# Performance work log

Hardware: AMD Instinct MI355X
Metric: run time of the kernel (lower is better)

The kernel has to match this reference:

```python
import jax, jax.numpy as jnp
import numpy as np

M, K, N = 8192, 4096, 4096
INT8_MAX = 127.0


def setup_inputs() -> dict:
    key = jax.random.key(0)
    k1, k2, k3, k4 = jax.random.split(key, 4)
    inp = jax.random.normal(k1, (M, K), dtype=jnp.float32)
    # int8 weight [out_features, in_features]
    weight = jax.random.randint(k2, (N, K), -128, 128, dtype=jnp.int32).astype(jnp.int8)
    # per-output-channel dequant scale
    weight_scale = jax.random.uniform(k3, (N,), dtype=jnp.float32, minval=1e-3, maxval=1e-2)
    bias = jax.random.normal(k4, (N,), dtype=jnp.float32) * 0.01
    return {"input": inp, "weight": weight, "weight_scale": weight_scale, "bias": bias}


def reference(input, weight, weight_scale, bias):
    # Dynamic per-token symmetric int8 quantization (scaled_int8_quant with
    # scale=None, azp=None, symmetric=True): scale_a = max|x| / 127 per row.
    absmax = jnp.max(jnp.abs(input), axis=-1, keepdims=True)  # [M, 1]
    scale_a = jnp.where(absmax > 0, absmax / INT8_MAX, jnp.float32(1.0))
    q = jnp.clip(jnp.round(input / scale_a), -128, 127).astype(jnp.int8)  # [M, K]
    # and per-column (weight_scale) dequant, plus bias, in input dtype.
    acc = jnp.matmul(q.astype(jnp.int32), weight.T.astype(jnp.int32))  # [M, N] int32
    out = acc.astype(jnp.float32) * scale_a * weight_scale[None, :] + bias[None, :]
    return out.astype(input.dtype)
```

## Files before the change

kernel.cpp:

```cpp
#include <hip/hip_runtime.h>
#include <cstdint>

typedef __attribute__((ext_vector_type(4))) int int32x4;
typedef __attribute__((ext_vector_type(16))) int int32x16;

#define GLOBAL_AS __attribute__((address_space(1)))
#define LDS_AS    __attribute__((address_space(3)))

__global__ __launch_bounds__(256) void pack_w(
    const int* __restrict__ w32, uint32_t* __restrict__ w8_as_u32)
{
    const size_t i = (size_t)blockIdx.x * 256 + threadIdx.x;
    const int4 v = ((const int4*)w32)[i];
    w8_as_u32[i] = (v.x & 0xff) | ((v.y & 0xff) << 8) |
                   ((v.z & 0xff) << 16) | ((uint32_t)(v.w & 0xff) << 24);
}

__global__ __launch_bounds__(256) void quant_rows(
    const float* __restrict__ in, int8_t* __restrict__ q,
    float* __restrict__ sa, int K)
{
    const int row = blockIdx.x;
    const float4* rp = (const float4*)(in + (size_t)row * K);
    const int t = threadIdx.x;

    float amax = 0.f;
    float4 v[4];
#pragma unroll
    for (int i = 0; i < 4; ++i) {
        v[i] = rp[t + (i << 8)];
        amax = fmaxf(amax,
               fmaxf(fmaxf(fabsf(v[i].x), fabsf(v[i].y)),
                     fmaxf(fabsf(v[i].z), fabsf(v[i].w))));
    }

#pragma unroll
    for (int off = 32; off; off >>= 1)
        amax = fmaxf(amax, __shfl_xor(amax, off));
    __shared__ float smax[4];
    if ((t & 63) == 0) smax[t >> 6] = amax;
    __syncthreads();
    amax = fmaxf(fmaxf(smax[0], smax[1]), fmaxf(smax[2], smax[3]));

    const float scale = (amax > 0.f) ? (amax / 127.f) : 1.f;
    if (t == 0) sa[row] = scale;
    const float rs = 1.f / scale;

    int* qrow = (int*)(q + (size_t)row * K);
#pragma unroll
    for (int i = 0; i < 4; ++i) {
        int a = __float2int_rn(v[i].x * rs);
        int b = __float2int_rn(v[i].y * rs);
        int c = __float2int_rn(v[i].z * rs);
        int d = __float2int_rn(v[i].w * rs);
        a = max(-128, min(127, a));
        b = max(-128, min(127, b));
        c = max(-128, min(127, c));
        d = max(-128, min(127, d));
        qrow[t + (i << 8)] = (a & 0xff) | ((b & 0xff) << 8) |
                             ((c & 0xff) << 16) | ((d & 0xff) << 24);
    }
}

__device__ __forceinline__ void async_load16(const int8_t* g, int8_t* lds) {
    __builtin_amdgcn_global_load_lds((const GLOBAL_AS char*)g,
                                     (LDS_AS char*)lds, 16, 0, 0);
}

__global__ __launch_bounds__(256, 1) void w8a8_gemm(
    const int8_t* __restrict__ Aq, const int8_t* __restrict__ W,
    const float* __restrict__ sa, const float* __restrict__ wsc,
    const float* __restrict__ bias, float* __restrict__ out,
    int M, int N, int K)
{
    __shared__ int8_t lds[4 * 32768];

    const int NB = N >> 8;
    const int nwg = gridDim.x;
    const int cpx = nwg >> 3;
    const int wg = (blockIdx.x & 7) * cpx + (blockIdx.x >> 3);
    const int bm = wg / NB, bn = wg % NB;

    const int t = threadIdx.x;
    const int lane = t & 63, wid = t >> 6;
    const int wr = wid >> 1, wc = wid & 1;
    const int l31 = lane & 31, h = lane >> 5;
    const int pswz = ((lane >> 1) ^ (lane >> 3)) & 3;

    const int srow = t >> 2;
    const int scol = (((t & 3) ^ ((t >> 3) & 3) ^ ((t >> 5) & 3)) << 4);
    const int8_t* gA = Aq + ((size_t)bm * 256 + srow) * (size_t)K + scol;
    const int8_t* gB = W  + ((size_t)bn * 256 + srow) * (size_t)K + scol;
    const size_t rstep = (size_t)64 * K;
    const size_t hstep = (size_t)128 * K;
    int8_t* ldsw = &lds[t * 16];

    auto stage = [&](int ring, int kbyte, int c) {
        const int8_t* s0 = (c < 2 ? gA : gB) + (size_t)(c & 1) * hstep + kbyte;
        int8_t* d0 = ldsw + ring * 32768 + (c >> 1) * 16384 + (c & 1) * 8192;
        async_load16(s0, d0);
        async_load16(s0 + rstep, d0 + 4096);
    };

    const int aoff = wr * 8192 + l31 * 64;
    const int boff = 16384 + wc * 8192 + l31 * 64;
    const int cs0 = ((0 + h) ^ pswz) << 4;
    const int cs1 = ((2 + h) ^ pswz) << 4;

    int32x16 acc[4][4];
#pragma unroll
    for (int m = 0; m < 4; ++m)
#pragma unroll
        for (int n = 0; n < 4; ++n)
#pragma unroll
            for (int rgi = 0; rgi < 16; ++rgi)
                acc[m][n][rgi] = 0;

    const int NT = K >> 6;

#pragma unroll
    for (int c = 0; c < 4; ++c) stage(0, 0, c);
#pragma unroll
    for (int c = 0; c < 4; ++c) stage(1, 64, c);
    asm volatile("s_waitcnt vmcnt(8)" ::: "memory");
    asm volatile("s_barrier" ::: "memory");

    for (int g = 0; g < NT; ++g) {
        const int rbase = (g & 3) * 32768;
        const int sring = (g + 2) & 3;
        const int skb = (g + 2) << 6;
        const bool do_stage = (g + 2) < NT;

        int32x4 a0[4], b0[4], a1[4], b1[4];
#pragma unroll
        for (int m = 0; m < 4; ++m)
            a0[m] = *(const int32x4*)&lds[rbase + aoff + m * 2048 + cs0];
#pragma unroll
        for (int n = 0; n < 4; ++n)
            b0[n] = *(const int32x4*)&lds[rbase + boff + n * 2048 + cs0];

        if (do_stage) {
#pragma unroll
            for (int c = 0; c < 4; ++c) stage(sring, skb, c);
        }

#pragma unroll
        for (int m = 0; m < 4; ++m)
            a1[m] = *(const int32x4*)&lds[rbase + aoff + m * 2048 + cs1];
#pragma unroll
        for (int n = 0; n < 4; ++n)
            b1[n] = *(const int32x4*)&lds[rbase + boff + n * 2048 + cs1];

#pragma unroll
        for (int m = 0; m < 4; ++m)
#pragma unroll
            for (int n = 0; n < 4; ++n)
                acc[m][n] = __builtin_amdgcn_mfma_i32_32x32x32_i8(
                    a0[m], b0[n], acc[m][n], 0, 0, 0);
#pragma unroll
        for (int m = 0; m < 4; ++m)
#pragma unroll
            for (int n = 0; n < 4; ++n)
                acc[m][n] = __builtin_amdgcn_mfma_i32_32x32x32_i8(
                    a1[m], b1[n], acc[m][n], 0, 0, 0);

        if (g < NT - 2)
            asm volatile("s_waitcnt vmcnt(8)" ::: "memory");
        else
            asm volatile("s_waitcnt vmcnt(0)" ::: "memory");
        asm volatile("s_barrier" ::: "memory");
    }

    const int col0 = bn * 256 + wc * 128 + l31;
    const int row00 = bm * 256 + wr * 128 + 4 * h;

#pragma unroll
    for (int m = 0; m < 4; ++m) {
        float sv[16];
#pragma unroll
        for (int rgi = 0; rgi < 16; ++rgi)
            sv[rgi] = sa[row00 + m * 32 + (rgi & 3) + 8 * (rgi >> 2)];
#pragma unroll
        for (int n = 0; n < 4; ++n) {
            const int col = col0 + n * 32;
            const float wn = wsc[col];
            const float bb = bias[col];
#pragma unroll
            for (int rgi = 0; rgi < 16; ++rgi) {
                const int row = row00 + m * 32 + (rgi & 3) + 8 * (rgi >> 2);
                out[(size_t)row * N + col] =
                    (float)acc[m][n][rgi] * sv[rgi] * wn + bb;
            }
        }
    }
}

extern "C" void kernel_launch(void* const* d_in, const int* in_sizes, int n_in,
                              void* d_out, int out_size, void* d_ws, size_t ws_size,
                              hipStream_t stream) {
    const float* inp  = (const float*)d_in[0];
    const int*   w32  = (const int*)d_in[1];
    const float* wsc  = (const float*)d_in[2];
    const float* bias = (const float*)d_in[3];
    float* out = (float*)d_out;

    const int N = in_sizes[2];
    const int K = in_sizes[1] / N;
    const int M = in_sizes[0] / K;

    int8_t* q  = (int8_t*)d_ws;
    float*  sa = (float*)((char*)d_ws + (size_t)M * K);
    int8_t* w8 = (int8_t*)((char*)d_ws + (size_t)M * K + (size_t)M * 4 + 256);

    const size_t nw4 = ((size_t)N * K) / 4;
    pack_w<<<(int)(nw4 / 256), 256, 0, stream>>>(w32, (uint32_t*)w8);

    quant_rows<<<M, 256, 0, stream>>>(inp, q, sa, K);

    const int nwg = (M / 256) * (N / 256);
    w8a8_gemm<<<nwg, 256, 0, stream>>>(q, w8, sa, wsc, bias, out, M, N, K);
}
```

Baseline: 195.7 us.

## Switch GEMM to double-buffered 128-K groups with conflict-free LDS layout

The 4-slot ring of 64-byte K tiles with XOR-swizzled LDS layout is replaced by a 2-slot double buffer that stages 128 bytes of K per group. The LDS layout is reorganised so each lane reads a contiguous 16-byte chunk (lane*16), which removes the swizzle arithmetic and aims for bank-conflict-free reads. Each barrier now covers twice the MFMA work, so there is less synchronisation overhead. In exchange, prefetch depth drops to one group and each iteration waits for all outstanding loads (vmcnt(0)), which could expose memory latency.

Result: slower. 243.9 us (+24.6%).

```diff
diff --git a/kernel.cpp b/kernel.cpp
--- a/kernel.cpp
+++ b/kernel.cpp
@@ -73,7 +73,7 @@
     const float* __restrict__ bias, float* __restrict__ out,
     int M, int N, int K)
 {
-    __shared__ int8_t lds[4 * 32768];
+    __shared__ int8_t lds[2 * 65536];
 
     const int NB = N >> 8;
     const int nwg = gridDim.x;
@@ -85,27 +85,31 @@
     const int lane = t & 63, wid = t >> 6;
     const int wr = wid >> 1, wc = wid & 1;
     const int l31 = lane & 31, h = lane >> 5;
-    const int pswz = ((lane >> 1) ^ (lane >> 3)) & 3;
-
-    const int srow = t >> 2;
-    const int scol = (((t & 3) ^ ((t >> 3) & 3) ^ ((t >> 5) & 3)) << 4);
+
+    const int srow = ((t >> 7) << 5) + (t & 31);
+    const int scol = ((((t >> 6) & 1) * 2 + ((t >> 5) & 1)) << 4);
     const int8_t* gA = Aq + ((size_t)bm * 256 + srow) * (size_t)K + scol;
     const int8_t* gB = W  + ((size_t)bn * 256 + srow) * (size_t)K + scol;
     const size_t rstep = (size_t)64 * K;
     const size_t hstep = (size_t)128 * K;
     int8_t* ldsw = &lds[t * 16];
 
-    auto stage = [&](int ring, int kbyte, int c) {
-        const int8_t* s0 = (c < 2 ? gA : gB) + (size_t)(c & 1) * hstep + kbyte;
-        int8_t* d0 = ldsw + ring * 32768 + (c >> 1) * 16384 + (c & 1) * 8192;
-        async_load16(s0, d0);
-        async_load16(s0 + rstep, d0 + 4096);
+    auto stage_group = [&](int slot, int kbyte) {
+#pragma unroll
+        for (int c = 0; c < 8; ++c) {
+            const int sub = c & 3;
+            const int kt = c >> 2;
+            const int8_t* s0 = (sub < 2 ? gA : gB) +
+                               (size_t)(sub & 1) * hstep + kbyte + kt * 64;
+            int8_t* d0 = ldsw + slot * 65536 + (sub >= 2 ? 32768 : 0) +
+                         kt * 16384 + (sub & 1) * 8192;
+            async_load16(s0, d0);
+            async_load16(s0 + rstep, d0 + 4096);
+        }
     };
 
-    const int aoff = wr * 8192 + l31 * 64;
-    const int boff = 16384 + wc * 8192 + l31 * 64;
-    const int cs0 = ((0 + h) ^ pswz) << 4;
-    const int cs1 = ((2 + h) ^ pswz) << 4;
+    const int aoff = wr * 8192 + lane * 16;
+    const int boff = 32768 + wc * 8192 + lane * 16;
 
     int32x16 acc[4][4];
 #pragma unroll
@@ -116,58 +120,46 @@
             for (int rgi = 0; rgi < 16; ++rgi)
                 acc[m][n][rgi] = 0;
 
-    const int NT = K >> 6;
-
-#pragma unroll
-    for (int c = 0; c < 4; ++c) stage(0, 0, c);
-#pragma unroll
-    for (int c = 0; c < 4; ++c) stage(1, 64, c);
-    asm volatile("s_waitcnt vmcnt(8)" ::: "memory");
+    const int NG = K >> 7;
+
+    stage_group(0, 0);
+    asm volatile("s_waitcnt vmcnt(0)" ::: "memory");
     asm volatile("s_barrier" ::: "memory");
 
-    for (int g = 0; g < NT; ++g) {
-        const int rbase = (g & 3) * 32768;
-        const int sring = (g + 2) & 3;
-        const int skb = (g + 2) << 6;
-        const bool do_stage = (g + 2) < NT;
-
-        int32x4 a0[4], b0[4], a1[4], b1[4];
-#pragma unroll
-        for (int m = 0; m < 4; ++m)
-            a0[m] = *(const int32x4*)&lds[rbase + aoff + m * 2048 + cs0];
-#pragma unroll
-        for (int n = 0; n < 4; ++n)
-            b0[n] = *(const int32x4*)&lds[rbase + boff + n * 2048 + cs0];
-
-        if (do_stage) {
-#pragma unroll
-            for (int c = 0; c < 4; ++c) stage(sring, skb, c);
+    for (int g = 0; g < NG; ++g) {
+        const int rbase = (g & 1) * 65536;
+
+        if (g + 1 < NG) stage_group((g + 1) & 1, (g + 1) << 7);
+
+#pragma unroll
+        for (int kt = 0; kt < 2; ++kt) {
+            const int tb = rbase + kt * 16384;
+            int32x4 a0[4], b0[4], a1[4], b1[4];
+#pragma unroll
+            for (int m = 0; m < 4; ++m) {
+                a0[m] = *(const int32x4*)&lds[tb + aoff + m * 2048];
+                a1[m] = *(const int32x4*)&lds[tb + aoff + m * 2048 + 1024];
+            }
+#pragma unroll
+            for (int n = 0; n < 4; ++n) {
+                b0[n] = *(const int32x4*)&lds[tb + boff + n * 2048];
+                b1[n] = *(const int32x4*)&lds[tb + boff + n * 2048 + 1024];
+            }
+#pragma unroll
+            for (int m = 0; m < 4; ++m)
+#pragma unroll
+                for (int n = 0; n < 4; ++n)
+                    acc[m][n] = __builtin_amdgcn_mfma_i32_32x32x32_i8(
+                        a0[m], b0[n], acc[m][n], 0, 0, 0);
+#pragma unroll
+            for (int m = 0; m < 4; ++m)
+#pragma unroll
+                for (int n = 0; n < 4; ++n)
+                    acc[m][n] = __builtin_amdgcn_mfma_i32_32x32x32_i8(
+                        a1[m], b1[n], acc[m][n], 0, 0, 0);
         }
 
-#pragma unroll
-        for (int m = 0; m < 4; ++m)
-            a1[m] = *(const int32x4*)&lds[rbase + aoff + m * 2048 + cs1];
-#pragma unroll
-        for (int n = 0; n < 4; ++n)
-            b1[n] = *(const int32x4*)&lds[rbase + boff + n * 2048 + cs1];
-
-#pragma unroll
-        for (int m = 0; m < 4; ++m)
-#pragma unroll
-            for (int n = 0; n < 4; ++n)
-                acc[m][n] = __builtin_amdgcn_mfma_i32_32x32x32_i8(
-                    a0[m], b0[n], acc[m][n], 0, 0, 0);
-#pragma unroll
-        for (int m = 0; m < 4; ++m)
-#pragma unroll
-            for (int n = 0; n < 4; ++n)
-                acc[m][n] = __builtin_amdgcn_mfma_i32_32x32x32_i8(
-                    a1[m], b1[n], acc[m][n], 0, 0, 0);
-
-        if (g < NT - 2)
-            asm volatile("s_waitcnt vmcnt(8)" ::: "memory");
-        else
-            asm volatile("s_waitcnt vmcnt(0)" ::: "memory");
+        asm volatile("s_waitcnt vmcnt(0)" ::: "memory");
         asm volatile("s_barrier" ::: "memory");
     }
 
```
